# Kernel optimization log

Hardware: AMD Instinct MI355X
Metric: run time of the kernel (lower is better)

The kernel has to match this reference:

```python
import jax, jax.numpy as jnp
import numpy as np

N_NODES = 50000
N_EDGES = 800000
IN_DIM = 128
OUT_DIM = 64


def setup_inputs() -> dict:
    key = jax.random.key(0)
    k1, k2, k3, k4, k5 = jax.random.split(key, 5)
    h = jax.random.normal(k1, (N_NODES, IN_DIM), dtype=jnp.float32)
    # Xavier-normal-ish scale for weights
    W_w = jax.random.normal(k2, (IN_DIM, OUT_DIM), dtype=jnp.float32) * (2.0 / (IN_DIM + OUT_DIM)) ** 0.5
    W_b = jnp.zeros((OUT_DIM,), dtype=jnp.float32)
    A_w = jax.random.normal(k3, (2 * OUT_DIM, 1), dtype=jnp.float32) * (2.0 / (2 * OUT_DIM + 1)) ** 0.5
    A_b = jnp.zeros((1,), dtype=jnp.float32)
    src = jax.random.randint(k4, (N_EDGES,), 0, N_NODES, dtype=jnp.int32)
    dst = jax.random.randint(k5, (N_EDGES,), 0, N_NODES, dtype=jnp.int32)
    return {"h": h, "W_w": W_w, "W_b": W_b, "A_w": A_w, "A_b": A_b, "src": src, "dst": dst}


def reference(h, W_w, W_b, A_w, A_b, src, dst):
    n = h.shape[0]
    # Node projection: Wh = W(h)
    Wh = h @ W_w + W_b  # [N, D]
    # Attention logit e_ij = LeakyReLU(A([Wh_i; Wh_j])), computed as node-level
    # partial scores gathered per edge (same math as concat-linear, far less traffic).
    a_dst = (Wh @ A_w[:OUT_DIM, 0])  # [N] -> contribution of Wh_i (dst)
    a_src = (Wh @ A_w[OUT_DIM:, 0])  # [N] -> contribution of Wh_j (src)
    e = jax.nn.leaky_relu(a_dst[dst] + a_src[src] + A_b[0], negative_slope=0.2)  # [E]
    # Segment softmax over incoming edges of each destination node (stable).
    m = jax.ops.segment_max(e, dst, num_segments=n)  # [N], -inf for isolated nodes
    m = jnp.where(jnp.isfinite(m), m, 0.0)
    ex = jnp.exp(e - m[dst])  # [E]
    den = jax.ops.segment_sum(ex, dst, num_segments=n)  # [N]
    alpha = ex / den[dst]  # [E]
    # Weighted scatter-sum aggregate: h_i = sum_j alpha_ij * Wh_j
    out = jax.ops.segment_sum(alpha[:, None] * Wh[src], dst, num_segments=n)  # [N, D]
    # Dropout (p=0.6) is identity in eval mode; omitted for determinism.
    return out
```

## Files before the change

### kernel.cpp

```cpp
#include <hip/hip_runtime.h>
#include <hip/hip_bf16.h>
#include <hip/hip_fp16.h>

#define IN_DIM 128
#define OUT_DIM 64
#define MAXDEG 64
#define CSTRIDE 16

typedef __attribute__((ext_vector_type(8))) short short8v;
typedef __attribute__((ext_vector_type(4))) float float4v;
typedef unsigned short ushort_t;
typedef unsigned int uint_t;

__device__ inline ushort_t f_to_bf16(float f) {
    uint_t x = __float_as_uint(f);
    uint_t r = (x + 0x7fffu + ((x >> 16) & 1u)) >> 16;
    return (ushort_t)r;
}

__global__ __launch_bounds__(256) void gat_fused(
    const float* __restrict__ h, const float* __restrict__ W,
    const float* __restrict__ Wb, const float* __restrict__ Aw,
    ushort_t* __restrict__ Whb, float* __restrict__ a_dst_arr,
    float* __restrict__ a_src_arr, int N,
    const int* __restrict__ src, const int* __restrict__ dst,
    int* __restrict__ cnt, uint_t* __restrict__ csr, int E, int HB)
{
    __shared__ ushort_t Wl[16 * 64 * 8];

    const int t = threadIdx.x;

    if ((int)blockIdx.x < HB) {
        int base = ((int)blockIdx.x * 256 + t) * 4;
        if (base + 4 <= E) {
            int4 d4 = *(const int4*)&dst[base];
            int4 s4 = *(const int4*)&src[base];
            int r0 = atomicAdd(&cnt[d4.x * CSTRIDE], 1);
            int r1 = atomicAdd(&cnt[d4.y * CSTRIDE], 1);
            int r2 = atomicAdd(&cnt[d4.z * CSTRIDE], 1);
            int r3 = atomicAdd(&cnt[d4.w * CSTRIDE], 1);
            if (r0 < MAXDEG) csr[d4.x * MAXDEG + r0] = (uint_t)s4.x;
            if (r1 < MAXDEG) csr[d4.y * MAXDEG + r1] = (uint_t)s4.y;
            if (r2 < MAXDEG) csr[d4.z * MAXDEG + r2] = (uint_t)s4.z;
            if (r3 < MAXDEG) csr[d4.w * MAXDEG + r3] = (uint_t)s4.w;
        } else {
            for (int e = base; e < E; e++) {
                int d = dst[e];
                int r = atomicAdd(&cnt[d * CSTRIDE], 1);
                if (r < MAXDEG) csr[d * MAXDEG + r] = (uint_t)src[e];
            }
        }
        return;
    }

    const int pb = (int)blockIdx.x - HB;
    {
        int f = t * 32;
        #pragma unroll
        for (int i = 0; i < 32; i++, f++) {
            int frag = f >> 9;
            int lane = (f >> 3) & 63;
            int j    = f & 7;
            int k    = (frag >> 2) * 32 + (lane >> 4) * 8 + j;
            int d    = (frag & 3) * 16 + (lane & 15);
            Wl[f] = f_to_bf16(W[k * OUT_DIM + d]);
        }
    }
    __syncthreads();

    const int wave  = t >> 6;
    const int lane  = t & 63;
    const int node0 = (pb * 4 + wave) * 16;
    if (node0 >= N) return;
    const int quad = lane >> 4;
    const int col  = lane & 15;

    const int rowc = min(node0 + col, N - 1);
    const float* __restrict__ arow = h + (size_t)rowc * IN_DIM;

    float4v acc[4];
    #pragma unroll
    for (int db = 0; db < 4; db++) acc[db] = (float4v){0.f, 0.f, 0.f, 0.f};

    #pragma unroll
    for (int kb = 0; kb < 4; kb++) {
        const float* ap = arow + kb * 32 + quad * 8;
        float4 a0 = *(const float4*)ap;
        float4 a1 = *(const float4*)(ap + 4);
        union { short8v v; ushort_t u[8]; } af;
        af.u[0] = f_to_bf16(a0.x); af.u[1] = f_to_bf16(a0.y);
        af.u[2] = f_to_bf16(a0.z); af.u[3] = f_to_bf16(a0.w);
        af.u[4] = f_to_bf16(a1.x); af.u[5] = f_to_bf16(a1.y);
        af.u[6] = f_to_bf16(a1.z); af.u[7] = f_to_bf16(a1.w);
        #pragma unroll
        for (int db = 0; db < 4; db++) {
            short8v bf = *(const short8v*)&Wl[(((kb << 2) | db) * 64 + lane) * 8];
            acc[db] = __builtin_amdgcn_mfma_f32_16x16x32_bf16(af.v, bf, acc[db], 0, 0, 0);
        }
    }

    float wbv[4], awd[4], aws[4];
    #pragma unroll
    for (int db = 0; db < 4; db++) {
        wbv[db] = Wb[db * 16 + col];
        awd[db] = Aw[db * 16 + col];
        aws[db] = Aw[OUT_DIM + db * 16 + col];
    }

    float pd[4] = {0.f, 0.f, 0.f, 0.f};
    float ps[4] = {0.f, 0.f, 0.f, 0.f};
    #pragma unroll
    for (int db = 0; db < 4; db++) {
        #pragma unroll
        for (int r = 0; r < 4; r++) {
            float v = acc[db][r] + wbv[db];
            int node = node0 + quad * 4 + r;
            if (node < N)
                Whb[(size_t)node * OUT_DIM + db * 16 + col] = f_to_bf16(v);
            pd[r] = fmaf(v, awd[db], pd[r]);
            ps[r] = fmaf(v, aws[db], ps[r]);
        }
    }
    #pragma unroll
    for (int r = 0; r < 4; r++) {
        float d_ = pd[r], s_ = ps[r];
        #pragma unroll
        for (int off = 1; off < 16; off <<= 1) {
            d_ += __shfl_xor(d_, off);
            s_ += __shfl_xor(s_, off);
        }
        int node = node0 + quad * 4 + r;
        if (col == 0 && node < N) {
            a_dst_arr[node] = d_;
            a_src_arr[node] = s_;
        }
    }
}

__global__ __launch_bounds__(256) void gat_agg(
    const int* __restrict__ cnt, const uint_t* __restrict__ csr,
    const uint_t* __restrict__ Whb2,
    const float* __restrict__ a_dst_arr, const float* __restrict__ a_src_arr,
    const float* __restrict__ Ab,
    float* __restrict__ out, int N)
{
    int node = (int)((blockIdx.x * blockDim.x + threadIdx.x) >> 6);
    int lane = threadIdx.x & 63;
    if (node >= N) return;
    int u   = __builtin_amdgcn_readfirstlane(node);
    int deg = min(cnt[u * CSTRIDE], MAXDEG);
    float ad = a_dst_arr[u] + Ab[0];
    const uint_t* __restrict__ seg = csr + (size_t)u * MAXDEG;

    const int el = lane >> 5;
    const int dl = lane & 31;

    float accx = 0.f, accy = 0.f, wsum = 0.f;

    int j = 0;
    for (; j + 8 <= deg; j += 8) {
        #pragma unroll
        for (int b = 0; b < 4; b++) {
            int   s = (int)seg[j + b * 2 + el];
            float v = ad + a_src_arr[s];
            v = (v > 0.0f) ? v : 0.2f * v;
            float w = __expf(v);
            uint_t p = Whb2[(size_t)s * 32 + dl];
            float fx = __uint_as_float(p << 16);
            float fy = __uint_as_float(p & 0xffff0000u);
            accx = fmaf(w, fx, accx);
            accy = fmaf(w, fy, accy);
            wsum += w;
        }
    }
    for (; j < deg; j += 2) {
        int e = j + el;
        if (e < deg) {
            int   s = (int)seg[e];
            float v = ad + a_src_arr[s];
            v = (v > 0.0f) ? v : 0.2f * v;
            float w = __expf(v);
            uint_t p = Whb2[(size_t)s * 32 + dl];
            float fx = __uint_as_float(p << 16);
            float fy = __uint_as_float(p & 0xffff0000u);
            accx = fmaf(w, fx, accx);
            accy = fmaf(w, fy, accy);
            wsum += w;
        }
    }

    accx += __shfl_xor(accx, 32);
    accy += __shfl_xor(accy, 32);
    wsum += __shfl_xor(wsum, 32);

    float inv = (deg > 0) ? 1.0f / wsum : 0.0f;
    if (lane < 32) {
        float2 o = make_float2(accx * inv, accy * inv);
        *(float2*)&out[(size_t)u * OUT_DIM + dl * 2] = o;
    }
}

extern "C" void kernel_launch(void* const* d_in, const int* in_sizes, int n_in,
                              void* d_out, int out_size, void* d_ws, size_t ws_size,
                              hipStream_t stream)
{
    const float* h   = (const float*)d_in[0];
    const float* W_w = (const float*)d_in[1];
    const float* W_b = (const float*)d_in[2];
    const float* A_w = (const float*)d_in[3];
    const float* A_b = (const float*)d_in[4];
    const int*   src = (const int*)d_in[5];
    const int*   dst = (const int*)d_in[6];
    float* out = (float*)d_out;

    const int N = in_sizes[0] / IN_DIM;
    const int E = in_sizes[5];

    ushort_t* Whb   = (ushort_t*)d_ws;
    float* a_dst_a  = (float*)(Whb + (size_t)N * OUT_DIM);
    float* a_src_a  = a_dst_a + N;
    int*   cnt      = (int*)(a_src_a + N);
    uint_t* csr     = (uint_t*)(cnt + (size_t)N * CSTRIDE);

    (void)hipMemsetAsync(cnt, 0, (size_t)N * CSTRIDE * sizeof(int), stream);

    {
        int HB = (E + 1023) / 1024;
        int waves = (N + 15) / 16;
        int PB = (waves + 3) / 4;
        gat_fused<<<HB + PB, 256, 0, stream>>>(h, W_w, W_b, A_w, Whb,
                                               a_dst_a, a_src_a, N,
                                               src, dst, cnt, csr, E, HB);
    }
    {
        int grid = (N + 3) / 4;
        gat_agg<<<grid, 256, 0, stream>>>(cnt, csr, (const uint_t*)Whb,
                                          a_dst_a, a_src_a, A_b, out, N);
    }
}
```

Measured before the change: 174.7 us.

## Pack degree counters densely and process four edges per wave with 8-byte gathers

```diff
diff --git a/kernel.cpp b/kernel.cpp
--- a/kernel.cpp
+++ b/kernel.cpp
@@ -5,7 +5,6 @@
 #define IN_DIM 128
 #define OUT_DIM 64
 #define MAXDEG 64
-#define CSTRIDE 16
 
 typedef __attribute__((ext_vector_type(8))) short short8v;
 typedef __attribute__((ext_vector_type(4))) float float4v;
@@ -35,10 +34,10 @@
         if (base + 4 <= E) {
             int4 d4 = *(const int4*)&dst[base];
             int4 s4 = *(const int4*)&src[base];
-            int r0 = atomicAdd(&cnt[d4.x * CSTRIDE], 1);
-            int r1 = atomicAdd(&cnt[d4.y * CSTRIDE], 1);
-            int r2 = atomicAdd(&cnt[d4.z * CSTRIDE], 1);
-            int r3 = atomicAdd(&cnt[d4.w * CSTRIDE], 1);
+            int r0 = atomicAdd(&cnt[d4.x], 1);
+            int r1 = atomicAdd(&cnt[d4.y], 1);
+            int r2 = atomicAdd(&cnt[d4.z], 1);
+            int r3 = atomicAdd(&cnt[d4.w], 1);
             if (r0 < MAXDEG) csr[d4.x * MAXDEG + r0] = (uint_t)s4.x;
             if (r1 < MAXDEG) csr[d4.y * MAXDEG + r1] = (uint_t)s4.y;
             if (r2 < MAXDEG) csr[d4.z * MAXDEG + r2] = (uint_t)s4.z;
@@ -46,7 +45,7 @@
         } else {
             for (int e = base; e < E; e++) {
                 int d = dst[e];
-                int r = atomicAdd(&cnt[d * CSTRIDE], 1);
+                int r = atomicAdd(&cnt[d], 1);
                 if (r < MAXDEG) csr[d * MAXDEG + r] = (uint_t)src[e];
             }
         }
@@ -148,55 +147,60 @@
     int lane = threadIdx.x & 63;
     if (node >= N) return;
     int u   = __builtin_amdgcn_readfirstlane(node);
-    int deg = min(cnt[u * CSTRIDE], MAXDEG);
+    int deg = min(cnt[u], MAXDEG);
     float ad = a_dst_arr[u] + Ab[0];
     const uint_t* __restrict__ seg = csr + (size_t)u * MAXDEG;
 
-    const int el = lane >> 5;
-    const int dl = lane & 31;
-
-    float accx = 0.f, accy = 0.f, wsum = 0.f;
+    const int el = lane >> 4;
+    const int dl = lane & 15;
+
+    float ax = 0.f, ay = 0.f, az = 0.f, aw = 0.f, wsum = 0.f;
 
     int j = 0;
-    for (; j + 8 <= deg; j += 8) {
+    for (; j + 16 <= deg; j += 16) {
         #pragma unroll
         for (int b = 0; b < 4; b++) {
-            int   s = (int)seg[j + b * 2 + el];
+            int   s = (int)seg[j + b * 4 + el];
             float v = ad + a_src_arr[s];
             v = (v > 0.0f) ? v : 0.2f * v;
             float w = __expf(v);
-            uint_t p = Whb2[(size_t)s * 32 + dl];
-            float fx = __uint_as_float(p << 16);
-            float fy = __uint_as_float(p & 0xffff0000u);
-            accx = fmaf(w, fx, accx);
-            accy = fmaf(w, fy, accy);
+            uint2 p = *(const uint2*)&Whb2[(size_t)s * 32 + dl * 2];
+            ax = fmaf(w, __uint_as_float(p.x << 16), ax);
+            ay = fmaf(w, __uint_as_float(p.x & 0xffff0000u), ay);
+            az = fmaf(w, __uint_as_float(p.y << 16), az);
+            aw = fmaf(w, __uint_as_float(p.y & 0xffff0000u), aw);
             wsum += w;
         }
     }
-    for (; j < deg; j += 2) {
+    for (; j < deg; j += 4) {
         int e = j + el;
         if (e < deg) {
             int   s = (int)seg[e];
             float v = ad + a_src_arr[s];
             v = (v > 0.0f) ? v : 0.2f * v;
             float w = __expf(v);
-            uint_t p = Whb2[(size_t)s * 32 + dl];
-            float fx = __uint_as_float(p << 16);
-            float fy = __uint_as_float(p & 0xffff0000u);
-            accx = fmaf(w, fx, accx);
-            accy = fmaf(w, fy, accy);
+            uint2 p = *(const uint2*)&Whb2[(size_t)s * 32 + dl * 2];
+            ax = fmaf(w, __uint_as_float(p.x << 16), ax);
+            ay = fmaf(w, __uint_as_float(p.x & 0xffff0000u), ay);
+            az = fmaf(w, __uint_as_float(p.y << 16), az);
+            aw = fmaf(w, __uint_as_float(p.y & 0xffff0000u), aw);
             wsum += w;
         }
     }
 
-    accx += __shfl_xor(accx, 32);
-    accy += __shfl_xor(accy, 32);
-    wsum += __shfl_xor(wsum, 32);
+    #pragma unroll
+    for (int off = 16; off < 64; off <<= 1) {
+        ax   += __shfl_xor(ax, off);
+        ay   += __shfl_xor(ay, off);
+        az   += __shfl_xor(az, off);
+        aw   += __shfl_xor(aw, off);
+        wsum += __shfl_xor(wsum, off);
+    }
 
     float inv = (deg > 0) ? 1.0f / wsum : 0.0f;
-    if (lane < 32) {
-        float2 o = make_float2(accx * inv, accy * inv);
-        *(float2*)&out[(size_t)u * OUT_DIM + dl * 2] = o;
+    if (lane < 16) {
+        float4 o = make_float4(ax * inv, ay * inv, az * inv, aw * inv);
+        *(float4*)&out[(size_t)u * OUT_DIM + dl * 4] = o;
     }
 }
 
@@ -220,9 +224,9 @@
     float* a_dst_a  = (float*)(Whb + (size_t)N * OUT_DIM);
     float* a_src_a  = a_dst_a + N;
     int*   cnt      = (int*)(a_src_a + N);
-    uint_t* csr     = (uint_t*)(cnt + (size_t)N * CSTRIDE);
-
-    (void)hipMemsetAsync(cnt, 0, (size_t)N * CSTRIDE * sizeof(int), stream);
+    uint_t* csr     = (uint_t*)(cnt + N);
+
+    (void)hipMemsetAsync(cnt, 0, (size_t)N * sizeof(int), stream);
 
     {
         int HB = (E + 1023) / 1024;
```

Result: no change. 178.0 us (+1.9%).
